# Kernel optimization log

Hardware: AMD Instinct MI355X
Metric: run time of the kernel (lower is better)

## Reference

```python
import jax, jax.numpy as jnp
import numpy as np

N = 32768          # tokens per modal
TOKEN_DIM = 1024
HID_DIM = 1024
SENSE_DIM = 256
K = 512            # centroids (shared size across modals)


def setup_inputs() -> dict:
    key = jax.random.key(0)
    ks = jax.random.split(key, 10)
    s = 0.02
    return {
        "text_emb": jax.random.normal(ks[0], (N, TOKEN_DIM), jnp.float32),
        "image_emb": jax.random.normal(ks[1], (N, TOKEN_DIM), jnp.float32),
        "text_W1": jax.random.normal(ks[2], (TOKEN_DIM, HID_DIM), jnp.float32) * s,
        "text_W2": jax.random.normal(ks[3], (HID_DIM, HID_DIM), jnp.float32) * s,
        "text_W3": jax.random.normal(ks[4], (HID_DIM, SENSE_DIM), jnp.float32) * s,
        "image_W1": jax.random.normal(ks[5], (TOKEN_DIM, HID_DIM), jnp.float32) * s,
        "image_W2": jax.random.normal(ks[6], (HID_DIM, HID_DIM), jnp.float32) * s,
        "image_W3": jax.random.normal(ks[7], (HID_DIM, SENSE_DIM), jnp.float32) * s,
        "centroids_raw": jax.random.uniform(ks[8], (K, SENSE_DIM), jnp.float32),
    }


def _sense_map(x, W1, W2, W3):
    # Linear(bias=False)+Tanh x3
    h = jnp.tanh(x @ W1)
    h = jnp.tanh(h @ W2)
    return jnp.tanh(h @ W3)  # [N, sense_dim]


def _assign(se, centroids):
    # squared distance [K, N] via expansion (same math as broadcast-subtract)
    c2 = jnp.sum(centroids * centroids, axis=1)[:, None]      # [K,1]
    e2 = jnp.sum(se * se, axis=1)[None, :]                     # [1,N]
    sqdist = c2 + e2 - 2.0 * (centroids @ se.T)                # [K,N]
    # torch argmax over (sqdist.T == min) picks first min -> argmin first occurrence
    return jnp.argmin(sqdist, axis=0)                          # [N] int


def reference(text_emb, image_emb, text_W1, text_W2, text_W3,
              image_W1, image_W2, image_W3, centroids_raw):
    centroids = jnp.tanh(centroids_raw)
    se_t = _sense_map(text_emb, text_W1, text_W2, text_W3)
    se_i = _sense_map(image_emb, image_W1, image_W2, image_W3)
    sc_t = _assign(se_t, centroids)
    sc_i = _assign(se_i, centroids)

    sense_embeddings = jnp.concatenate([se_t, se_i], axis=0)   # [2N, sense_dim]
    sense_class = jnp.concatenate([sc_t, sc_i], axis=0)        # [2N]
    word_class = jnp.concatenate([jnp.zeros((N,), jnp.int32),
                                  jnp.ones((N,), jnp.int32)])

    # ragged per-sense grouping represented jit-compatibly as a stable sort
    # permutation + per-sense counts (per modal)
    order_t = jnp.argsort(sc_t, stable=True)
    order_i = jnp.argsort(sc_i, stable=True)
    counts_t = jnp.zeros((K,), jnp.int32).at[sc_t].add(1)
    counts_i = jnp.zeros((K,), jnp.int32).at[sc_i].add(1)

    return (centroids, sense_embeddings, word_class, sense_class,
            order_t, counts_t, order_i, counts_i)
```

## Files before the change

### kernel.cpp

```cpp
#include <hip/hip_runtime.h>
#include <math.h>

#define NTOK 32768
typedef unsigned short ushort_t;

#define OFF_CENT 0
#define OFF_SE   131072
#define OFF_WC   16908288
#define OFF_SC   16973824
#define OFF_OT   17039360
#define OFF_CT   17072128
#define OFF_OI   17072640
#define OFF_CI   17105408

typedef __attribute__((ext_vector_type(8))) short short8v;
typedef __attribute__((ext_vector_type(4))) float f32x4;

__device__ __forceinline__ float dot4(float4 a, float4 b){
    return a.x*b.x + a.y*b.y + a.z*b.z + a.w*b.w;
}

__device__ __forceinline__ ushort_t f2bf(float x){
    unsigned int u = __float_as_uint(x);
    unsigned int r = (u + 0x7fffu + ((u >> 16) & 1u)) >> 16;
    return (ushort_t)r;
}
__device__ __forceinline__ float bf2f(ushort_t h){
    return __uint_as_float(((unsigned int)h) << 16);
}

__device__ __forceinline__ void gload16(const void* g, void* l){
    __builtin_amdgcn_global_load_lds(
        (const __attribute__((address_space(1))) void*)g,
        (__attribute__((address_space(3))) void*)l,
        16, 0, 0);
}

__global__ __launch_bounds__(64) void k_cent(const float* __restrict__ raw,
                                             float* __restrict__ out,
                                             float* __restrict__ c2,
                                             ushort_t* __restrict__ ch,
                                             ushort_t* __restrict__ cl)
{
    int c = blockIdx.x, l = threadIdx.x;
    float4 v = *(const float4*)(raw + (size_t)c*256 + l*4);
    float4 t;
    t.x = tanhf(v.x); t.y = tanhf(v.y); t.z = tanhf(v.z); t.w = tanhf(v.w);
    *(float4*)(out + OFF_CENT + (size_t)c*256 + l*4) = t;
    ushort4 h = make_ushort4(f2bf(t.x), f2bf(t.y), f2bf(t.z), f2bf(t.w));
    ushort4 lo = make_ushort4(f2bf(t.x - bf2f(h.x)), f2bf(t.y - bf2f(h.y)),
                              f2bf(t.z - bf2f(h.z)), f2bf(t.w - bf2f(h.w)));
    *(ushort4*)(ch + (size_t)c*256 + l*4) = h;
    *(ushort4*)(cl + (size_t)c*256 + l*4) = lo;
    float s = dot4(t, t);
    #pragma unroll
    for (int off = 32; off > 0; off >>= 1) s += __shfl_down(s, off);
    if (l == 0) c2[c] = s;
}

__global__ __launch_bounds__(256) void k_wc(float* __restrict__ out)
{
    int g = blockIdx.x*256 + threadIdx.x;
    float v = (g*4 < NTOK) ? 0.f : 1.f;
    float4* p = (float4*)(out + OFF_WC);
    p[g] = make_float4(v, v, v, v);
}

__global__ __launch_bounds__(256) void k_esplit(const float* __restrict__ x,
                                                ushort_t* __restrict__ hi,
                                                ushort_t* __restrict__ lo,
                                                long n4)
{
    long g = (long)blockIdx.x*256 + threadIdx.x;
    if (g >= n4) return;
    float4 v = ((const float4*)x)[g];
    ushort_t h0 = f2bf(v.x), h1 = f2bf(v.y), h2 = f2bf(v.z), h3 = f2bf(v.w);
    ushort4 h = make_ushort4(h0, h1, h2, h3);
    ushort4 l = make_ushort4(f2bf(v.x - bf2f(h0)), f2bf(v.y - bf2f(h1)),
                             f2bf(v.z - bf2f(h2)), f2bf(v.w - bf2f(h3)));
    ((ushort4*)hi)[g] = h;
    ((ushort4*)lo)[g] = l;
}

__global__ __launch_bounds__(256) void k_wsplit(const float* __restrict__ W,
                                                ushort_t* __restrict__ Wt_hi,
                                                ushort_t* __restrict__ Wt_lo,
                                                int K, int N)
{
    __shared__ float t[32][33];
    int k0 = blockIdx.y*32, n0 = blockIdx.x*32;
    int tx = threadIdx.x & 31, ty = threadIdx.x >> 5;
    #pragma unroll
    for (int r = 0; r < 4; ++r)
        t[ty + r*8][tx] = W[(size_t)(k0 + ty + r*8)*N + n0 + tx];
    __syncthreads();
    #pragma unroll
    for (int r = 0; r < 4; ++r) {
        int n = ty + r*8;
        float x = t[tx][n];
        ushort_t h = f2bf(x);
        Wt_hi[(size_t)(n0+n)*K + k0 + tx] = h;
        Wt_lo[(size_t)(n0+n)*K + k0 + tx] = f2bf(x - bf2f(h));
    }
}

__global__ __launch_bounds__(512, 2) void k_gemm_mfma256(
    const ushort_t* __restrict__ A_hi, const ushort_t* __restrict__ Bt_hi,
    ushort_t* __restrict__ C_hi, ushort_t* __restrict__ C_lo,
    unsigned aDelta, unsigned bDelta, int N)
{
    __shared__ ushort_t lds[65536];

    const int tid  = threadIdx.x;
    const int wave = tid >> 6, lane = tid & 63;
    const int wr = wave >> 2, wc = wave & 3;
    const int fr = lane & 15, fq = lane >> 4;

    int nwg = gridDim.x;
    int id = blockIdx.x;
    if (!(nwg & 7)) { int cpx = nwg >> 3; id = (id & 7)*cpx + (id >> 3); }
    const int nx = N >> 8;
    const int n0 = (id % nx) * 256;
    const int m0 = (id / nx) * 256;

    const int srow0 = tid >> 2;
    const int qx = (tid & 3) ^ ((srow0 >> 1) & 3);

    const unsigned offA0 = (unsigned)(m0 + srow0) * 1024u + (unsigned)qx * 8u;
    const unsigned offB0 = (unsigned)(n0 + srow0) * 1024u + (unsigned)qx * 8u;
    const ushort_t* pA0  = A_hi + offA0;
    const ushort_t* pA1  = pA0 + 131072u;
    const ushort_t* pA0l = pA0 + aDelta;
    const ushort_t* pA1l = pA1 + aDelta;
    const ushort_t* pB0  = Bt_hi + offB0;
    const ushort_t* pB1  = pB0 + 131072u;
    const ushort_t* pB0l = pB0 + bDelta;
    const ushort_t* pB1l = pB1 + bDelta;
    const unsigned ldsS0 = (unsigned)wave * 512u;
    const unsigned ldsS1 = ldsS0 + 4096u;

    const unsigned fb = (unsigned)fr*32u + (unsigned)((fq ^ ((fr >> 1) & 3)) * 8);
    const ushort_t* p0 = lds + fb;
    const ushort_t* p1 = p0 + 32768u;

    f32x4 acc[8][4] = {};

#define STG(KT, WB) { \
    unsigned wb_ = (unsigned)(WB) * 32768u; \
    gload16(pA0  + (KT), lds + wb_ +           ldsS0); \
    gload16(pA1  + (KT), lds + wb_ +           ldsS1); \
    gload16(pA0l + (KT), lds + wb_ +  8192u +  ldsS0); \
    gload16(pA1l + (KT), lds + wb_ +  8192u +  ldsS1); \
    gload16(pB0  + (KT), lds + wb_ + 16384u +  ldsS0); \
    gload16(pB1  + (KT), lds + wb_ + 16384u +  ldsS1); \
    gload16(pB0l + (KT), lds + wb_ + 24576u +  ldsS0); \
    gload16(pB1l + (KT), lds + wb_ + 24576u +  ldsS1); \
}

#define RA(P, hl, i) (*(const short8v*)((P) + (hl)*8192u + (unsigned)wr*4096u + (unsigned)(i)*512u))
#define RB(P, hl, j) (*(const short8v*)((P) + 16384u + (hl)*8192u + (unsigned)wc*2048u + (unsigned)(j)*512u))

#define MM16(A8, B8, C4) __builtin_amdgcn_mfma_f32_16x16x32_bf16(A8, B8, C4, 0, 0, 0)

    STG(0, 0);
    __syncthreads();

    #pragma unroll 1
    for (int kt = 0; kt < 1024; kt += 32) {
        const int par = (kt >> 5) & 1;
        const ushort_t* cp = par ? p1 : p0;

        if (kt + 32 < 1024) STG(kt + 32, par ^ 1);

        short8v bh0 = RB(cp,0,0), bl0 = RB(cp,1,0);
        short8v bh1 = RB(cp,0,1), bl1 = RB(cp,1,1);
        short8v bh2 = RB(cp,0,2), bl2 = RB(cp,1,2);
        short8v bh3 = RB(cp,0,3), bl3 = RB(cp,1,3);

        __builtin_amdgcn_s_setprio(1);
        #pragma unroll
        for (int i = 0; i < 8; ++i) {
            short8v ah = RA(cp,0,i), al = RA(cp,1,i);
            acc[i][0] = MM16(ah, bh0, acc[i][0]);
            acc[i][1] = MM16(ah, bh1, acc[i][1]);
            acc[i][2] = MM16(ah, bh2, acc[i][2]);
            acc[i][3] = MM16(ah, bh3, acc[i][3]);
            acc[i][0] = MM16(ah, bl0, acc[i][0]);
            acc[i][1] = MM16(ah, bl1, acc[i][1]);
            acc[i][2] = MM16(ah, bl2, acc[i][2]);
            acc[i][3] = MM16(ah, bl3, acc[i][3]);
            acc[i][0] = MM16(al, bh0, acc[i][0]);
            acc[i][1] = MM16(al, bh1, acc[i][1]);
            acc[i][2] = MM16(al, bh2, acc[i][2]);
            acc[i][3] = MM16(al, bh3, acc[i][3]);
        }
        __builtin_amdgcn_s_setprio(0);

        __syncthreads();
    }

    #pragma unroll
    for (int i = 0; i < 8; ++i)
        #pragma unroll
        for (int j = 0; j < 4; ++j)
            #pragma unroll
            for (int r = 0; r < 4; ++r) {
                int row = m0 + wr*128 + i*16 + fq*4 + r;
                int col = n0 + wc*64 + j*16 + fr;
                float t = tanhf(acc[i][j][r]);
                size_t idx = (size_t)row*N + col;
                ushort_t h = f2bf(t);
                C_hi[idx] = h;
                C_lo[idx] = f2bf(t - bf2f(h));
            }
#undef STG
#undef RA
#undef RB
#undef MM16
}

__global__ __launch_bounds__(256, 2) void k_gemm_mfma(
    const ushort_t* __restrict__ A_hi, const ushort_t* __restrict__ A_lo,
    const ushort_t* __restrict__ Bt_hi, const ushort_t* __restrict__ Bt_lo,
    ushort_t* __restrict__ C_hi, ushort_t* __restrict__ C_lo,
    float* __restrict__ Cf,
    int N)
{
    const int K = 1024;
    __shared__ ushort_t lds[16384];

    const int tid  = threadIdx.x;
    const int wave = tid >> 6, lane = tid & 63;
    const int wr = wave >> 1, wc = wave & 1;

    int nwg = gridDim.x * gridDim.y;
    int id = blockIdx.y * gridDim.x + blockIdx.x;
    if (!(nwg & 7)) { int cpx = nwg >> 3; id = (id & 7)*cpx + (id >> 3); }
    const int m0 = (id / gridDim.x) * 128, n0 = (id % gridDim.x) * 128;

    f32x4 acc[4][4] = {};

    int srow[2], sq[2], slbase[2];
    #pragma unroll
    for (int r = 0; r < 2; ++r) {
        int row = wave*32 + r*16 + (lane >> 2);
        srow[r]   = row;
        sq[r]     = (lane & 3) ^ ((row >> 1) & 3);
        slbase[r] = wave*1024 + r*512;
    }

    const int fr = lane & 15, fq = lane >> 4;

    for (int kt = 0; kt < K; kt += 32) {
        __syncthreads();
        #pragma unroll
        for (int r = 0; r < 2; ++r) {
            size_t ga = (size_t)(m0 + srow[r]) * K + kt + sq[r]*8;
            size_t gb = (size_t)(n0 + srow[r]) * K + kt + sq[r]*8;
            gload16(A_hi  + ga, lds          + slbase[r]);
            gload16(A_lo  + ga, lds + 4096   + slbase[r]);
            gload16(Bt_hi + gb, lds + 8192   + slbase[r]);
            gload16(Bt_lo + gb, lds + 12288  + slbase[r]);
        }
        __syncthreads();

        short8v ah[4], al[4], bh[4], bl[4];
        #pragma unroll
        for (int i = 0; i < 4; ++i) {
            int rowa = wr*64 + i*16 + fr;
            int offa = rowa*32 + ((fq ^ ((rowa >> 1) & 3)) * 8);
            ah[i] = *(const short8v*)(lds + offa);
            al[i] = *(const short8v*)(lds + 4096 + offa);
            int rowb = wc*64 + i*16 + fr;
            int offb = rowb*32 + ((fq ^ ((rowb >> 1) & 3)) * 8);
            bh[i] = *(const short8v*)(lds + 8192 + offb);
            bl[i] = *(const short8v*)(lds + 12288 + offb);
        }
        #pragma unroll
        for (int i = 0; i < 4; ++i)
            #pragma unroll
            for (int j = 0; j < 4; ++j) {
                acc[i][j] = __builtin_amdgcn_mfma_f32_16x16x32_bf16(ah[i], bh[j], acc[i][j], 0, 0, 0);
                acc[i][j] = __builtin_amdgcn_mfma_f32_16x16x32_bf16(ah[i], bl[j], acc[i][j], 0, 0, 0);
                acc[i][j] = __builtin_amdgcn_mfma_f32_16x16x32_bf16(al[i], bh[j], acc[i][j], 0, 0, 0);
            }
    }

    #pragma unroll
    for (int i = 0; i < 4; ++i)
        #pragma unroll
        for (int j = 0; j < 4; ++j)
            #pragma unroll
            for (int r = 0; r < 4; ++r) {
                int row = m0 + wr*64 + i*16 + fq*4 + r;
                int col = n0 + wc*64 + j*16 + fr;
                float t = tanhf(acc[i][j][r]);
                size_t idx = (size_t)row*N + col;
                if (Cf) Cf[idx] = t;
                if (C_hi) {
                    ushort_t h = f2bf(t);
                    C_hi[idx] = h;
                    C_lo[idx] = f2bf(t - bf2f(h));
                }
            }
}

__global__ __launch_bounds__(256) void k_assign_mfma(
    const ushort_t* __restrict__ SEh, const ushort_t* __restrict__ SEl,
    const ushort_t* __restrict__ ch, const ushort_t* __restrict__ cl,
    const float* __restrict__ c2,
    int* __restrict__ sc, float* __restrict__ out_w)
{
    __shared__ ushort_t lds[16384];
    __shared__ float c2s[512];
    __shared__ float redD[128][2];
    __shared__ int   redI[128][2];

    const int modal = blockIdx.y;
    const int t0 = blockIdx.x * 128;
    const int tid  = threadIdx.x;
    const int wave = tid >> 6, lane = tid & 63;
    const int wr = wave >> 1, wc = wave & 1;
    const int fr = lane & 15, fq = lane >> 4;

    const ushort_t* seh = SEh + (size_t)modal * NTOK * 256;
    const ushort_t* sel = SEl + (size_t)modal * NTOK * 256;

    c2s[tid] = c2[tid];
    c2s[tid + 256] = c2[tid + 256];

    int srow[2], sq[2], slbase[2];
    #pragma unroll
    for (int r = 0; r < 2; ++r) {
        int row = wave*32 + r*16 + (lane >> 2);
        srow[r]   = row;
        sq[r]     = (lane & 3) ^ ((row >> 1) & 3);
        slbase[r] = wave*1024 + r*512;
    }

    float bd[16]; int bi[16];
    #pragma unroll
    for (int s = 0; s < 16; ++s) { bd[s] = 3.4e38f; bi[s] = 0; }

    for (int j = 0; j < 4; ++j) {
        f32x4 acc[4][4] = {};
        for (int kt = 0; kt < 256; kt += 32) {
            __syncthreads();
            #pragma unroll
            for (int r = 0; r < 2; ++r) {
                size_t ga = (size_t)(t0 + srow[r]) * 256 + kt + sq[r]*8;
                size_t gc = (size_t)(j*128 + srow[r]) * 256 + kt + sq[r]*8;
                gload16(seh + ga, lds          + slbase[r]);
                gload16(sel + ga, lds + 4096   + slbase[r]);
                gload16(ch  + gc, lds + 8192   + slbase[r]);
                gload16(cl  + gc, lds + 12288  + slbase[r]);
            }
            __syncthreads();

            short8v ah[4], al[4], bh[4], bl[4];
            #pragma unroll
            for (int i = 0; i < 4; ++i) {
                int rowa = wr*64 + i*16 + fr;
                int offa = rowa*32 + ((fq ^ ((rowa >> 1) & 3)) * 8);
                ah[i] = *(const short8v*)(lds + offa);
                al[i] = *(const short8v*)(lds + 4096 + offa);
                int rowb = wc*64 + i*16 + fr;
                int offb = rowb*32 + ((fq ^ ((rowb >> 1) & 3)) * 8);
                bh[i] = *(const short8v*)(lds + 8192 + offb);
                bl[i] = *(const short8v*)(lds + 12288 + offb);
            }
            #pragma unroll
            for (int i = 0; i < 4; ++i)
                #pragma unroll
                for (int jj = 0; jj < 4; ++jj) {
                    acc[i][jj] = __builtin_amdgcn_mfma_f32_16x16x32_bf16(ah[i], bh[jj], acc[i][jj], 0, 0, 0);
                    acc[i][jj] = __builtin_amdgcn_mfma_f32_16x16x32_bf16(ah[i], bl[jj], acc[i][jj], 0, 0, 0);
                    acc[i][jj] = __builtin_amdgcn_mfma_f32_16x16x32_bf16(al[i], bh[jj], acc[i][jj], 0, 0, 0);
                }
        }
        #pragma unroll
        for (int i = 0; i < 4; ++i)
            #pragma unroll
            for (int jj = 0; jj < 4; ++jj) {
                int col = j*128 + wc*64 + jj*16 + fr;
                float cc = c2s[col];
                #pragma unroll
                for (int r = 0; r < 4; ++r) {
                    float d = cc - 2.f * acc[i][jj][r];
                    int s = i*4 + r;
                    if (d < bd[s]) { bd[s] = d; bi[s] = col; }
                }
            }
    }

    #pragma unroll
    for (int s = 0; s < 16; ++s) {
        #pragma unroll
        for (int off = 1; off < 16; off <<= 1) {
            float od = __shfl_xor(bd[s], off);
            int   oi = __shfl_xor(bi[s], off);
            if (od < bd[s] || (od == bd[s] && oi < bi[s])) { bd[s] = od; bi[s] = oi; }
        }
    }
    if (fr == 0) {
        #pragma unroll
        for (int i = 0; i < 4; ++i)
            #pragma unroll
            for (int r = 0; r < 4; ++r) {
                int tl = wr*64 + i*16 + fq*4 + r;
                redD[tl][wc] = bd[i*4 + r];
                redI[tl][wc] = bi[i*4 + r];
            }
    }
    __syncthreads();
    if (tid < 128) {
        float d0 = redD[tid][0], d1 = redD[tid][1];
        int   i0 = redI[tid][0], i1 = redI[tid][1];
        if (d1 < d0 || (d1 == d0 && i1 < i0)) { d0 = d1; i0 = i1; }
        int g = t0 + tid;
        sc[modal*NTOK + g] = i0;
        out_w[OFF_SC + (size_t)modal*NTOK + g] = (float)i0;
    }
}

__global__ __launch_bounds__(256) void k_assign(
    const float* __restrict__ out_ro,
    const float* __restrict__ c2,
    int* __restrict__ sc,
    float* __restrict__ out_w)
{
    const int modal = blockIdx.y;
    const int tok0 = blockIdx.x * 64;
    const float* se   = out_ro + OFF_SE + (size_t)modal * NTOK * 256;
    const float* cent = out_ro + OFF_CENT;

    __shared__ float4 se4[64][64];
    __shared__ float4 ct4[64][64];

    const int tid = threadIdx.x;
    const int tt = tid & 15, cc = tid >> 4;

    {
        int rbase = tid >> 6;
        int d4 = tid & 63;
        #pragma unroll
        for (int i = 0; i < 16; ++i) {
            int t = i*4 + rbase;
            float4 v = *(const float4*)(se + (size_t)(tok0 + t)*256 + d4*4);
            se4[t][d4 ^ (t >> 2)] = v;
        }
    }
    __syncthreads();

    float e2r[4];
    #pragma unroll
    for (int k2 = 0; k2 < 4; ++k2) {
        float s = 0.f;
        for (int d4 = 0; d4 < 64; ++d4) {
            float4 v = se4[4*tt + k2][d4 ^ tt];
            s += dot4(v, v);
        }
        e2r[k2] = s;
    }

    float bd[4]; int bi[4];
    #pragma unroll
    for (int k2 = 0; k2 < 4; ++k2) { bd[k2] = 3.4e38f; bi[k2] = 0; }

    for (int ctile = 0; ctile < 8; ++ctile) {
        int c0 = ctile * 64;
        {
            int rbase = tid >> 6;
            int d4 = tid & 63;
            #pragma unroll
            for (int i = 0; i < 16; ++i) {
                int r = i*4 + rbase;
                float4 v = *(const float4*)(cent + (size_t)(c0 + r)*256 + d4*4);
                ct4[r][d4 ^ (r >> 2)] = v;
            }
        }
        __syncthreads();

        float accd[4][4];
        #pragma unroll
        for (int a = 0; a < 4; ++a)
            #pragma unroll
            for (int b = 0; b < 4; ++b) accd[a][b] = 0.f;

        for (int d4 = 0; d4 < 64; ++d4) {
            float4 sv[4], cv[4];
            #pragma unroll
            for (int k2 = 0; k2 < 4; ++k2) sv[k2] = se4[4*tt + k2][d4 ^ tt];
            #pragma unroll
            for (int jx = 0; jx < 4; ++jx) cv[jx] = ct4[4*cc + jx][d4 ^ cc];
            #pragma unroll
            for (int k2 = 0; k2 < 4; ++k2)
                #pragma unroll
                for (int jx = 0; jx < 4; ++jx)
                    accd[k2][jx] += dot4(sv[k2], cv[jx]);
        }

        #pragma unroll
        for (int jx = 0; jx < 4; ++jx) {
            int cidx = c0 + 4*cc + jx;
            float cj = c2[cidx];
            #pragma unroll
            for (int k2 = 0; k2 < 4; ++k2) {
                float d = cj + e2r[k2] - 2.f * accd[k2][jx];
                if (d < bd[k2]) { bd[k2] = d; bi[k2] = cidx; }
            }
        }
        __syncthreads();
    }

    float* red_d = (float*)ct4;
    int*   red_i = (int*)ct4 + 64*17;
    #pragma unroll
    for (int k2 = 0; k2 < 4; ++k2) {
        red_d[(4*tt + k2)*17 + cc] = bd[k2];
        red_i[(4*tt + k2)*17 + cc] = bi[k2];
    }
    __syncthreads();
    if (tid < 64) {
        float b = red_d[tid*17]; int ix = red_i[tid*17];
        #pragma unroll
        for (int q = 1; q < 16; ++q) {
            float d = red_d[tid*17 + q]; int i2 = red_i[tid*17 + q];
            if (d < b || (d == b && i2 < ix)) { b = d; ix = i2; }
        }
        int g = tok0 + tid;
        sc[modal*NTOK + g] = ix;
        out_w[OFF_SC + (size_t)modal*NTOK + g] = (float)ix;
    }
}

__global__ __launch_bounds__(256) void k_hist(const int* __restrict__ sc,
                                              int* __restrict__ blockHist)
{
    int modal = blockIdx.y, blk = blockIdx.x, tid = threadIdx.x;
    __shared__ int h[512];
    h[tid] = 0; h[tid + 256] = 0;
    __syncthreads();
    atomicAdd(&h[sc[modal*NTOK + blk*256 + tid]], 1);
    __syncthreads();
    int base = (modal*128 + blk) * 512;
    blockHist[base + tid]       = h[tid];
    blockHist[base + tid + 256] = h[tid + 256];
}

__global__ __launch_bounds__(512) void k_scan(const int* __restrict__ blockHist,
                                              int* __restrict__ blockBase,
                                              int* __restrict__ classBase,
                                              float* __restrict__ out)
{
    int modal = blockIdx.x;
    int c = threadIdx.x;
    int run = 0;
    for (int b = 0; b < 128; ++b) {
        int idx = (modal*128 + b)*512 + c;
        blockBase[idx] = run;
        run += blockHist[idx];
    }
    float* cnt = out + (modal ? OFF_CI : OFF_CT);
    cnt[c] = (float)run;

    __shared__ int s[512];
    s[c] = run;
    __syncthreads();
    int total = run;
    for (int off = 1; off < 512; off <<= 1) {
        int v = 0;
        if (c >= off) v = s[c - off];
        __syncthreads();
        s[c] += v;
        __syncthreads();
    }
    classBase[modal*512 + c] = s[c] - total;
}

__global__ __launch_bounds__(256) void k_scatter(const int* __restrict__ sc,
                                                 const int* __restrict__ blockBase,
                                                 const int* __restrict__ classBase,
                                                 float* __restrict__ out)
{
    int modal = blockIdx.y, blk = blockIdx.x, tid = threadIdx.x;
    __shared__ int cls[256];
    int t = blk*256 + tid;
    int c = sc[modal*NTOK + t];
    cls[tid] = c;
    __syncthreads();
    int rank = 0;
    for (int j = 0; j < tid; ++j) rank += (cls[j] == c) ? 1 : 0;
    int pos = classBase[modal*512 + c] + blockBase[(modal*128 + blk)*512 + c] + rank;
    float* oo = out + (modal ? OFF_OI : OFF_OT);
    oo[pos] = (float)t;
}

extern "C" void kernel_launch(void* const* d_in, const int* in_sizes, int n_in,
                              void* d_out, int out_size, void* d_ws, size_t ws_size,
                              hipStream_t stream)
{
    const float* text_emb  = (const float*)d_in[0];
    const float* image_emb = (const float*)d_in[1];
    const float* W[2][3] = {
        {(const float*)d_in[2], (const float*)d_in[3], (const float*)d_in[4]},
        {(const float*)d_in[5], (const float*)d_in[6], (const float*)d_in[7]}
    };
    const float* cent_raw = (const float*)d_in[8];
    float* out = (float*)d_out;
    char* w = (char*)d_ws;

    int*   sc        = (int*)w;
    int*   blockHist = (int*)(w + 0x40000);
    int*   blockBase = (int*)(w + 0xC0000);
    int*   classBase = (int*)(w + 0x140000);
    float* c2        = (float*)(w + 0x141000);
    ushort_t* cent_h = (ushort_t*)(w + 0x142000);
    ushort_t* cent_l = (ushort_t*)(w + 0x182000);

    ushort_t* wreg = (ushort_t*)(w + 0x200000);
    const size_t WM = 4*1048576 + 2*262144;

    ushort_t* SEh = (ushort_t*)(w + 0x1400000);
    ushort_t* SEl = (ushort_t*)(w + 0x3400000);

    bool mfmaAssign = true;
    size_t actoff = 0x5400000;
    int Mc = 0;
    for (int c = NTOK; c >= 128; c >>= 1)
        if (actoff + (size_t)c*8192 <= ws_size) { Mc = c; break; }
    if (Mc == 0) {
        mfmaAssign = false;
        actoff = 0x1400000;
        for (int c = NTOK; c >= 128; c >>= 1)
            if (actoff + (size_t)c*8192 <= ws_size) { Mc = c; break; }
        if (Mc == 0) Mc = 128;
    }
    ushort_t* act = (ushort_t*)(w + actoff);
    const bool big = (Mc % 256 == 0);

    k_cent<<<dim3(512), dim3(64), 0, stream>>>(cent_raw, out, c2, cent_h, cent_l);
    k_wc  <<<dim3(64),  dim3(256), 0, stream>>>(out);

    for (int m = 0; m < 2; ++m) {
        const float* emb = m ? image_emb : text_emb;
        ushort_t* w1h = wreg + (size_t)m*WM;
        ushort_t* w1l = w1h + 1048576;
        ushort_t* w2h = w1l + 1048576;
        ushort_t* w2l = w2h + 1048576;
        ushort_t* w3h = w2l + 1048576;
        ushort_t* w3l = w3h + 262144;

        k_wsplit<<<dim3(32, 32), dim3(256), 0, stream>>>(W[m][0], w1h, w1l, 1024, 1024);
        k_wsplit<<<dim3(32, 32), dim3(256), 0, stream>>>(W[m][1], w2h, w2l, 1024, 1024);
        k_wsplit<<<dim3(8,  32), dim3(256), 0, stream>>>(W[m][2], w3h, w3l, 1024, 256);

        ushort_t* Ah = act;
        ushort_t* Al = Ah + (size_t)Mc*1024;
        ushort_t* Hh = Al + (size_t)Mc*1024;
        ushort_t* Hl = Hh + (size_t)Mc*1024;

        for (int s0 = 0; s0 < NTOK; s0 += Mc) {
            long n4 = (long)Mc*1024/4;
            k_esplit<<<dim3((unsigned)((n4 + 255)/256)), dim3(256), 0, stream>>>(
                emb + (size_t)s0*1024, Ah, Al, n4);
            if (big) {
                k_gemm_mfma256<<<dim3((Mc/256)*4), dim3(512), 0, stream>>>(
                    Ah, w1h, Hh, Hl, (unsigned)Mc*1024u, 1048576u, 1024);
                k_gemm_mfma256<<<dim3((Mc/256)*4), dim3(512), 0, stream>>>(
                    Hh, w2h, Ah, Al, (unsigned)Mc*1024u, 1048576u, 1024);
            } else {
                k_gemm_mfma<<<dim3(8, Mc/128), dim3(256), 0, stream>>>(
                    Ah, Al, w1h, w1l, Hh, Hl, nullptr, 1024);
                k_gemm_mfma<<<dim3(8, Mc/128), dim3(256), 0, stream>>>(
                    Hh, Hl, w2h, w2l, Ah, Al, nullptr, 1024);
            }
            ushort_t* seh_ptr = mfmaAssign ? SEh + ((size_t)m*NTOK + s0)*256 : nullptr;
            ushort_t* sel_ptr = mfmaAssign ? SEl + ((size_t)m*NTOK + s0)*256 : nullptr;
            k_gemm_mfma<<<dim3(2, Mc/128), dim3(256), 0, stream>>>(
                Ah, Al, w3h, w3l, seh_ptr, sel_ptr,
                out + OFF_SE + ((size_t)m*NTOK + s0)*256, 256);
        }
    }

    if (mfmaAssign) {
        k_assign_mfma<<<dim3(256, 2), dim3(256), 0, stream>>>(
            SEh, SEl, cent_h, cent_l, c2, sc, out);
    } else {
        k_assign<<<dim3(512, 2), dim3(256), 0, stream>>>(out, c2, sc, out);
    }
    k_hist   <<<dim3(128, 2), dim3(256), 0, stream>>>(sc, blockHist);
    k_scan   <<<dim3(2),      dim3(512), 0, stream>>>(blockHist, blockBase, classBase, out);
    k_scatter<<<dim3(128, 2), dim3(256), 0, stream>>>(sc, blockBase, classBase, out);
}
```

Measured before the change: 1.088 ms.

## Fuse fp32-to-bf16 hi/lo split of embeddings into first-layer GEMM

Adds a first-layer GEMM kernel that reads fp32 embeddings directly from global memory, splits them into bf16 hi/lo in registers, and writes them to LDS. The separate k_esplit pass and its intermediate activation buffer round trip are skipped on the big path. It also moves the async stage prefetch in the existing 256-tile GEMM to after the B-fragment LDS reads. The fused kernel does the conversion inside the main loop using plain register loads rather than async LDS loads, which may add latency and register pressure.

Result: faster. 1.045 ms (-4.0%).

```diff
diff --git a/kernel.cpp b/kernel.cpp
--- a/kernel.cpp
+++ b/kernel.cpp
@@ -34,6 +34,16 @@
         (const __attribute__((address_space(1))) void*)g,
         (__attribute__((address_space(3))) void*)l,
         16, 0, 0);
+}
+
+__device__ __forceinline__ void cvt8(float4 a, float4 b, short8v& h, short8v& l){
+    float x[8] = {a.x, a.y, a.z, a.w, b.x, b.y, b.z, b.w};
+    #pragma unroll
+    for (int i = 0; i < 8; ++i) {
+        ushort_t hh = f2bf(x[i]);
+        h[i] = (short)hh;
+        l[i] = (short)f2bf(x[i] - bf2f(hh));
+    }
 }
 
 __global__ __launch_bounds__(64) void k_cent(const float* __restrict__ raw,
@@ -102,6 +112,144 @@
         Wt_hi[(size_t)(n0+n)*K + k0 + tx] = h;
         Wt_lo[(size_t)(n0+n)*K + k0 + tx] = f2bf(x - bf2f(h));
     }
+}
+
+__global__ __launch_bounds__(512, 2) void k_gemm_l1(
+    const float* __restrict__ Af, const ushort_t* __restrict__ Bt_hi,
+    ushort_t* __restrict__ C_hi, ushort_t* __restrict__ C_lo,
+    unsigned bDelta, int N)
+{
+    __shared__ ushort_t lds[65536];
+
+    const int tid  = threadIdx.x;
+    const int wave = tid >> 6, lane = tid & 63;
+    const int wr = wave >> 2, wc = wave & 3;
+    const int fr = lane & 15, fq = lane >> 4;
+
+    int nwg = gridDim.x;
+    int id = blockIdx.x;
+    if (!(nwg & 7)) { int cpx = nwg >> 3; id = (id & 7)*cpx + (id >> 3); }
+    const int nx = N >> 8;
+    const int n0 = (id % nx) * 256;
+    const int m0 = (id / nx) * 256;
+
+    const int srow0 = tid >> 2;
+    const int qx = (tid & 3) ^ ((srow0 >> 1) & 3);
+
+    const float* fA0 = Af + (size_t)(m0 + srow0) * 1024 + qx*8;
+    const float* fA1 = fA0 + 131072;
+    const unsigned offB0 = (unsigned)(n0 + srow0) * 1024u + (unsigned)qx * 8u;
+    const ushort_t* pB0  = Bt_hi + offB0;
+    const ushort_t* pB1  = pB0 + 131072u;
+    const ushort_t* pB0l = pB0 + bDelta;
+    const ushort_t* pB1l = pB1 + bDelta;
+    const unsigned ldsS0 = (unsigned)wave * 512u;
+    const unsigned ldsS1 = ldsS0 + 4096u;
+    const unsigned wOff  = ldsS0 + (unsigned)lane * 8u;
+
+    const unsigned fb = (unsigned)fr*32u + (unsigned)((fq ^ ((fr >> 1) & 3)) * 8);
+    const ushort_t* p0 = lds + fb;
+    const ushort_t* p1 = p0 + 32768u;
+
+    f32x4 acc[8][4] = {};
+
+#define STGB(KT, WB) { \
+    unsigned wb_ = (unsigned)(WB) * 32768u; \
+    gload16(pB0  + (KT), lds + wb_ + 16384u + ldsS0); \
+    gload16(pB1  + (KT), lds + wb_ + 16384u + ldsS1); \
+    gload16(pB0l + (KT), lds + wb_ + 24576u + ldsS0); \
+    gload16(pB1l + (KT), lds + wb_ + 24576u + ldsS1); \
+}
+#define RA1(P, hl, i) (*(const short8v*)((P) + (hl)*8192u + (unsigned)wr*4096u + (unsigned)(i)*512u))
+#define RB1(P, hl, j) (*(const short8v*)((P) + 16384u + (hl)*8192u + (unsigned)wc*2048u + (unsigned)(j)*512u))
+#define MM16(A8, B8, C4) __builtin_amdgcn_mfma_f32_16x16x32_bf16(A8, B8, C4, 0, 0, 0)
+
+    {
+        float4 a00 = *(const float4*)(fA0);
+        float4 a01 = *(const float4*)(fA0 + 4);
+        float4 a10 = *(const float4*)(fA1);
+        float4 a11 = *(const float4*)(fA1 + 4);
+        STGB(0, 0);
+        short8v h0, l0, h1, l1;
+        cvt8(a00, a01, h0, l0);
+        cvt8(a10, a11, h1, l1);
+        *(short8v*)(lds + wOff)          = h0;
+        *(short8v*)(lds + 4096u + wOff)  = h1;
+        *(short8v*)(lds + 8192u + wOff)  = l0;
+        *(short8v*)(lds + 12288u + wOff) = l1;
+    }
+    __syncthreads();
+
+    #pragma unroll 1
+    for (int kt = 0; kt < 1024; kt += 32) {
+        const int par = (kt >> 5) & 1;
+        const ushort_t* cp = par ? p1 : p0;
+        const bool pf = (kt + 32) < 1024;
+
+        float4 a00, a01, a10, a11;
+        if (pf) {
+            a00 = *(const float4*)(fA0 + kt + 32);
+            a01 = *(const float4*)(fA0 + kt + 36);
+            a10 = *(const float4*)(fA1 + kt + 32);
+            a11 = *(const float4*)(fA1 + kt + 36);
+            STGB(kt + 32, par ^ 1);
+        }
+
+        short8v bh0 = RB1(cp,0,0), bl0 = RB1(cp,1,0);
+        short8v bh1 = RB1(cp,0,1), bl1 = RB1(cp,1,1);
+        short8v bh2 = RB1(cp,0,2), bl2 = RB1(cp,1,2);
+        short8v bh3 = RB1(cp,0,3), bl3 = RB1(cp,1,3);
+
+        __builtin_amdgcn_s_setprio(1);
+        #pragma unroll
+        for (int i = 0; i < 8; ++i) {
+            short8v ah = RA1(cp,0,i), al = RA1(cp,1,i);
+            acc[i][0] = MM16(ah, bh0, acc[i][0]);
+            acc[i][1] = MM16(ah, bh1, acc[i][1]);
+            acc[i][2] = MM16(ah, bh2, acc[i][2]);
+            acc[i][3] = MM16(ah, bh3, acc[i][3]);
+            acc[i][0] = MM16(ah, bl0, acc[i][0]);
+            acc[i][1] = MM16(ah, bl1, acc[i][1]);
+            acc[i][2] = MM16(ah, bl2, acc[i][2]);
+            acc[i][3] = MM16(ah, bl3, acc[i][3]);
+            acc[i][0] = MM16(al, bh0, acc[i][0]);
+            acc[i][1] = MM16(al, bh1, acc[i][1]);
+            acc[i][2] = MM16(al, bh2, acc[i][2]);
+            acc[i][3] = MM16(al, bh3, acc[i][3]);
+        }
+        __builtin_amdgcn_s_setprio(0);
+
+        if (pf) {
+            unsigned wb = (unsigned)(par ^ 1) * 32768u;
+            short8v h0, l0, h1, l1;
+            cvt8(a00, a01, h0, l0);
+            cvt8(a10, a11, h1, l1);
+            *(short8v*)(lds + wb + wOff)          = h0;
+            *(short8v*)(lds + wb + 4096u + wOff)  = h1;
+            *(short8v*)(lds + wb + 8192u + wOff)  = l0;
+            *(short8v*)(lds + wb + 12288u + wOff) = l1;
+        }
+        __syncthreads();
+    }
+
+    #pragma unroll
+    for (int i = 0; i < 8; ++i)
+        #pragma unroll
+        for (int j = 0; j < 4; ++j)
+            #pragma unroll
+            for (int r = 0; r < 4; ++r) {
+                int row = m0 + wr*128 + i*16 + fq*4 + r;
+                int col = n0 + wc*64 + j*16 + fr;
+                float t = tanhf(acc[i][j][r]);
+                size_t idx = (size_t)row*N + col;
+                ushort_t h = f2bf(t);
+                C_hi[idx] = h;
+                C_lo[idx] = f2bf(t - bf2f(h));
+            }
+#undef STGB
+#undef RA1
+#undef RB1
+#undef MM16
 }
 
 __global__ __launch_bounds__(512, 2) void k_gemm_mfma256(
@@ -156,10 +304,8 @@
     gload16(pB0l + (KT), lds + wb_ + 24576u +  ldsS0); \
     gload16(pB1l + (KT), lds + wb_ + 24576u +  ldsS1); \
 }
-
 #define RA(P, hl, i) (*(const short8v*)((P) + (hl)*8192u + (unsigned)wr*4096u + (unsigned)(i)*512u))
 #define RB(P, hl, j) (*(const short8v*)((P) + 16384u + (hl)*8192u + (unsigned)wc*2048u + (unsigned)(j)*512u))
-
 #define MM16(A8, B8, C4) __builtin_amdgcn_mfma_f32_16x16x32_bf16(A8, B8, C4, 0, 0, 0)
 
     STG(0, 0);
@@ -170,12 +316,12 @@
         const int par = (kt >> 5) & 1;
         const ushort_t* cp = par ? p1 : p0;
 
-        if (kt + 32 < 1024) STG(kt + 32, par ^ 1);
-
         short8v bh0 = RB(cp,0,0), bl0 = RB(cp,1,0);
         short8v bh1 = RB(cp,0,1), bl1 = RB(cp,1,1);
         short8v bh2 = RB(cp,0,2), bl2 = RB(cp,1,2);
         short8v bh3 = RB(cp,0,3), bl3 = RB(cp,1,3);
+
+        if (kt + 32 < 1024) STG(kt + 32, par ^ 1);
 
         __builtin_amdgcn_s_setprio(1);
         #pragma unroll
@@ -661,15 +807,15 @@
         ushort_t* Hl = Hh + (size_t)Mc*1024;
 
         for (int s0 = 0; s0 < NTOK; s0 += Mc) {
-            long n4 = (long)Mc*1024/4;
-            k_esplit<<<dim3((unsigned)((n4 + 255)/256)), dim3(256), 0, stream>>>(
-                emb + (size_t)s0*1024, Ah, Al, n4);
             if (big) {
-                k_gemm_mfma256<<<dim3((Mc/256)*4), dim3(512), 0, stream>>>(
-                    Ah, w1h, Hh, Hl, (unsigned)Mc*1024u, 1048576u, 1024);
+                k_gemm_l1<<<dim3((Mc/256)*4), dim3(512), 0, stream>>>(
+                    emb + (size_t)s0*1024, w1h, Hh, Hl, 1048576u, 1024);
                 k_gemm_mfma256<<<dim3((Mc/256)*4), dim3(512), 0, stream>>>(
                     Hh, w2h, Ah, Al, (unsigned)Mc*1024u, 1048576u, 1024);
             } else {
+                long n4 = (long)Mc*1024/4;
+                k_esplit<<<dim3((unsigned)((n4 + 255)/256)), dim3(256), 0, stream>>>(
+                    emb + (size_t)s0*1024, Ah, Al, n4);
                 k_gemm_mfma<<<dim3(8, Mc/128), dim3(256), 0, stream>>>(
                     Ah, Al, w1h, w1l, Hh, Hl, nullptr, 1024);
                 k_gemm_mfma<<<dim3(8, Mc/128), dim3(256), 0, stream>>>(
```
